# Optimization experiments

Hardware: AMD Instinct MI355X
Metric: run time of the kernel (lower is better)

## Reference

```python
import jax, jax.numpy as jnp
import numpy as np

B, NQ, T, D, H, L = 2, 4, 1024, 1024, 16, 8
CARD, N_COND, COND_D, WIN = 1024, 64, 768, 5
DFF = 4 * D


def _ln(x, g, b):
    m = jnp.mean(x, axis=-1, keepdims=True)
    v = jnp.var(x, axis=-1, keepdims=True)
    return (x - m) * jax.lax.rsqrt(v + 1e-5) * g + b


def _mha(qx, kx, vx, Wq, bq, Wk, bk, Wv, bv, Wo, bo, mask):
    # qx:(B,Tq,D) kx/vx:(B,Tk,*)
    Bq, Tq = qx.shape[0], qx.shape[1]
    Tk = kx.shape[1]
    hd = D // H
    q = (qx @ Wq + bq).reshape(Bq, Tq, H, hd)
    k = (kx @ Wk + bk).reshape(Bq, Tk, H, hd)
    v = (vx @ Wv + bv).reshape(Bq, Tk, H, hd)
    s = jnp.einsum('bthd,bshd->bhts', q, k) / jnp.sqrt(jnp.float32(hd))
    if mask is not None:
        s = s + mask  # additive banded mask (0 in-band, -inf outside)
    p = jax.nn.softmax(s, axis=-1)
    o = jnp.einsum('bhts,bshd->bthd', p, v).reshape(Bq, Tq, D)
    return o @ Wo + bo


def _pos_emb(t, d):
    # matches get_sinusoidal_positional_embeddings: interleaved sin/cos
    i = jnp.arange(d // 2, dtype=jnp.float32) * 2.0
    p = jnp.arange(t, dtype=jnp.float32)[:, None]
    theta = p / (10000.0 ** (i / d))[None, :]  # (t, d/2)
    return jnp.stack([jnp.sin(theta), jnp.cos(theta)], axis=-1).reshape(t, d)[None]


def _band_mask(t, w):
    # magnet_restricted_att_mask with shift=0: log(tril(triu(1, -w), w))
    idx = jnp.arange(t)
    dlt = idx[None, :] - idx[:, None]
    return jnp.where((dlt >= -w) & (dlt <= w), 0.0, -jnp.inf).astype(jnp.float32)


def _forward(x, cond, emb,
             ln1_g, ln1_b, sWq, sbq, sWk, sbk, sWv, sbv, sWo, sbo,
             ln2_g, ln2_b, cWq, cbq, cWk, cbk, cWv, cbv, cWo, cbo,
             ln3_g, ln3_b, W1, b1, W2, b2, out_g, out_b, headW, headb):
    # multi-codebook embedding sum: (B,NQ,T) -> (B,T,D)
    h = emb[0][x[:, 0]]
    for q in range(1, NQ):
        h = h + emb[q][x[:, q]]
    h = h + _pos_emb(T, D).astype(h.dtype)
    mask = _band_mask(T, WIN)
    for l in range(L):
        sin = _ln(h, ln1_g[l], ln1_b[l])
        h = h + _mha(sin, sin, sin, sWq[l], sbq[l], sWk[l], sbk[l],
                     sWv[l], sbv[l], sWo[l], sbo[l], mask)
        cin = _ln(h, ln2_g[l], ln2_b[l])
        h = h + _mha(cin, cond, cond, cWq[l], cbq[l], cWk[l], cbk[l],
                     cWv[l], cbv[l], cWo[l], cbo[l], None)
        fin = _ln(h, ln3_g[l], ln3_b[l])
        h = h + (jax.nn.gelu(fin @ W1[l] + b1[l], approximate=True) @ W2[l] + b2[l])
    h = _ln(h, out_g, out_b)
    # per-codebook heads -> (B, NQ, T, CARD)
    return jnp.einsum('btd,qdk->bqtk', h, headW) + headb[None, :, None, :]


def setup_inputs() -> dict:
    key = jax.random.key(0)
    ks = iter(jax.random.split(key, 40))
    s = 0.02
    nrm = lambda shape: jax.random.normal(next(ks), shape, dtype=jnp.float32) * s
    inp = {}
    inp['x'] = jax.random.randint(next(ks), (B, NQ, T), 0, CARD + 1)
    inp['cond'] = jax.random.normal(next(ks), (B, N_COND, COND_D), dtype=jnp.float32)
    inp['emb'] = nrm((NQ, CARD + 1, D))
    for nm in ('ln1', 'ln2', 'ln3'):
        inp[nm + '_g'] = jnp.ones((L, D), jnp.float32)
        inp[nm + '_b'] = jnp.zeros((L, D), jnp.float32)
    # self-attn projections
    inp['sWq'], inp['sWk'], inp['sWv'], inp['sWo'] = (nrm((L, D, D)) for _ in range(4))
    inp['sbq'] = jnp.zeros((L, D), jnp.float32); inp['sbk'] = jnp.zeros((L, D), jnp.float32)
    inp['sbv'] = jnp.zeros((L, D), jnp.float32); inp['sbo'] = jnp.zeros((L, D), jnp.float32)
    # cross-attn projections (k/v act on cond_dim)
    inp['cWq'] = nrm((L, D, D)); inp['cWk'] = nrm((L, COND_D, D))
    inp['cWv'] = nrm((L, COND_D, D)); inp['cWo'] = nrm((L, D, D))
    inp['cbq'] = jnp.zeros((L, D), jnp.float32); inp['cbk'] = jnp.zeros((L, D), jnp.float32)
    inp['cbv'] = jnp.zeros((L, D), jnp.float32); inp['cbo'] = jnp.zeros((L, D), jnp.float32)
    inp['W1'] = nrm((L, D, DFF)); inp['b1'] = jnp.zeros((L, DFF), jnp.float32)
    inp['W2'] = nrm((L, DFF, D)); inp['b2'] = jnp.zeros((L, D), jnp.float32)
    inp['out_g'] = jnp.ones((D,), jnp.float32); inp['out_b'] = jnp.zeros((D,), jnp.float32)
    inp['headW'] = nrm((NQ, D, CARD)); inp['headb'] = jnp.zeros((NQ, CARD), jnp.float32)
    return inp


def reference(x, cond, emb,
              ln1_g, ln1_b, sWq, sbq, sWk, sbk, sWv, sbv, sWo, sbo,
              ln2_g, ln2_b, cWq, cbq, cWk, cbk, cWv, cbv, cWo, cbo,
              ln3_g, ln3_b, W1, b1, W2, b2, out_g, out_b, headW, headb):
    return _forward(x, cond, emb,
                    ln1_g, ln1_b, sWq, sbq, sWk, sbk, sWv, sbv, sWo, sbo,
                    ln2_g, ln2_b, cWq, cbq, cWk, cbk, cWv, cbv, cWo, cbo,
                    ln3_g, ln3_b, W1, b1, W2, b2, out_g, out_b, headW, headb)
```

## Files before the change

kernel.cpp:

```cpp
#include <hip/hip_runtime.h>
#include <math.h>

#define BATCH   2
#define NQ_CB   4
#define T_SEQ   1024
#define DMODEL  1024
#define NHEAD   16
#define HDIM    64
#define NLAYER  8
#define CARD_SZ 1024
#define NCOND   64
#define CONDD   768
#define DFF_SZ  4096
#define WIN     5

typedef __attribute__((ext_vector_type(8))) short bf16x8;
typedef __attribute__((ext_vector_type(4))) float f32x4;
typedef unsigned short ushortx;

__device__ inline short f2bf(float f) {
  union { float f; unsigned u; } c;
  c.f = f;
  unsigned r = (c.u + 0x7FFFu + ((c.u >> 16) & 1u)) >> 16;
  return (short)r;
}
__device__ inline float bf2f(unsigned short u) {
  union { unsigned u; float f; } c;
  c.u = ((unsigned)u) << 16;
  return c.f;
}

__device__ inline void gld_lds16(const void* g, void* s) {
  __builtin_amdgcn_global_load_lds(
      (const __attribute__((address_space(1))) void*)g,
      (__attribute__((address_space(3))) void*)s, 16, 0, 0);
}

__global__ __launch_bounds__(256) void pack_kernel(
    const float* __restrict__ src, short* __restrict__ dst, int K, int N)
{
  size_t matoff = (size_t)blockIdx.z * K * N;
  src += matoff; dst += matoff;
  int gid = blockIdx.x * 256 + threadIdx.x;
  int slab = gid >> 6, cell = gid & 63;
  int KT = K >> 5;
  int ng = slab / KT, kt = slab - ng * KT;
  int n = ng * 16 + (cell & 15);
  int k = kt * 32 + (cell >> 4) * 8;
  bf16x8 pk;
#pragma unroll
  for (int j = 0; j < 8; ++j) pk[j] = f2bf(src[(size_t)(k + j) * N + n]);
  *(bf16x8*)&dst[(size_t)gid * 8] = pk;
}

__global__ __launch_bounds__(256) void embed_kernel(
    const int* __restrict__ x, const float* __restrict__ emb,
    float* __restrict__ h)
{
  int bt = blockIdx.x;
  int b = bt >> 10, t = bt & (T_SEQ - 1);
  int tid = threadIdx.x;
  float4 acc = make_float4(0.f, 0.f, 0.f, 0.f);
#pragma unroll
  for (int q = 0; q < NQ_CB; ++q) {
    int idx = x[(b * NQ_CB + q) * T_SEQ + t];
    const float4* er =
        (const float4*)(emb + ((size_t)q * (CARD_SZ + 1) + idx) * DMODEL);
    float4 e = er[tid];
    acc.x += e.x; acc.y += e.y; acc.z += e.z; acc.w += e.w;
  }
  int d0 = tid * 4;
  float c = -logf(10000.f) * (2.f / (float)DMODEL);
  float th0 = (float)t * expf(c * (float)(d0 >> 1));
  float th1 = (float)t * expf(c * (float)((d0 + 2) >> 1));
  acc.x += sinf(th0); acc.y += cosf(th0);
  acc.z += sinf(th1); acc.w += cosf(th1);
  ((float4*)(h + (size_t)bt * DMODEL))[tid] = acc;
}

__global__ __launch_bounds__(256) void ln_kernel(
    const float* __restrict__ x, const float* __restrict__ g,
    const float* __restrict__ b, ushortx* __restrict__ y)
{
  int row = blockIdx.x;
  int tid = threadIdx.x;
  const float4* xr = (const float4*)(x + (size_t)row * DMODEL);
  float4 v = xr[tid];
  float s  = v.x + v.y + v.z + v.w;
  float ss = v.x * v.x + v.y * v.y + v.z * v.z + v.w * v.w;
#pragma unroll
  for (int off = 32; off; off >>= 1) {
    s  += __shfl_xor(s, off, 64);
    ss += __shfl_xor(ss, off, 64);
  }
  __shared__ float sh_s[4], sh_ss[4];
  int w = tid >> 6;
  if ((tid & 63) == 0) { sh_s[w] = s; sh_ss[w] = ss; }
  __syncthreads();
  s  = sh_s[0] + sh_s[1] + sh_s[2] + sh_s[3];
  ss = sh_ss[0] + sh_ss[1] + sh_ss[2] + sh_ss[3];
  float mean = s * (1.f / DMODEL);
  float var  = ss * (1.f / DMODEL) - mean * mean;
  float rstd = rsqrtf(var + 1e-5f);
  float4 gv = ((const float4*)g)[tid];
  float4 bv = ((const float4*)b)[tid];
  ushort4 o;
  o.x = (ushortx)f2bf((v.x - mean) * rstd * gv.x + bv.x);
  o.y = (ushortx)f2bf((v.y - mean) * rstd * gv.y + bv.y);
  o.z = (ushortx)f2bf((v.z - mean) * rstd * gv.z + bv.z);
  o.w = (ushortx)f2bf((v.w - mean) * rstd * gv.w + bv.w);
  *(ushort4*)(y + (size_t)row * DMODEL + tid * 4) = o;
}

#define FL_GELU  1
#define FL_REMAP 2
#define FL_OBF16 4

template <int MW, int ABF16>
__global__ __launch_bounds__(256, 2) void gemm_pk(
    const void* __restrict__ Ain,
    const short* __restrict__ Wp0, const short* __restrict__ Wp1,
    const short* __restrict__ Wp2, long wstride, int nw,
    const float* __restrict__ b0, const float* __restrict__ b1,
    const float* __restrict__ b2, long bstride,
    const float* __restrict__ resid,
    void* __restrict__ C0v, void* __restrict__ C1v, void* __restrict__ C2v,
    long cstride,
    int M, int N, int K, int flags)
{
  const int BM = MW * 32;
  __shared__ __align__(16) short Als[BM * 32];
  __shared__ __align__(16) short Bls[128 * 32];

  int tid = threadIdx.x;
  int z = blockIdx.z;
  int w = z % nw, li = z / nw;
  const short* Wp = (w == 0 ? Wp0 : (w == 1 ? Wp1 : Wp2)) + (size_t)li * wstride;
  const float* bias = (w == 0 ? b0 : (w == 1 ? b1 : b2)) + (size_t)li * bstride;
  char* Cb = (char*)(w == 0 ? C0v : (w == 1 ? C1v : C2v)) + (size_t)li * cstride;

  int bm = blockIdx.y * BM;
  int bn = blockIdx.x * 128;
  int wave = tid >> 6, lane = tid & 63;
  int wm = (wave >> 1) * (MW * 16);
  int wn = (wave & 1) * 64;
  int KT = K >> 5;

  f32x4 acc[MW][4];
#pragma unroll
  for (int i = 0; i < MW; ++i)
#pragma unroll
    for (int j = 0; j < 4; ++j) {
      acc[i][j][0] = 0.f; acc[i][j][1] = 0.f;
      acc[i][j][2] = 0.f; acc[i][j][3] = 0.f;
    }

  for (int kt = 0; kt < KT; ++kt) {
    int k0 = kt * 32;
#pragma unroll
    for (int i = 0; i < 2; ++i) {
      int g = wave * 2 + i;
      const short* src = Wp + ((size_t)((bn >> 4) + g) * KT + kt) * 512 + lane * 8;
      gld_lds16(src, &Bls[g * 512]);
    }
    if (ABF16) {
      const ushortx* A16 = (const ushortx*)Ain;
#pragma unroll
      for (int i = 0; i < (MW * 2 + 3) / 4; ++i) {
        int g = wave + i * 4;
        if (g < MW * 2) {
          const ushortx* src =
              A16 + (size_t)(bm + g * 16 + (lane & 15)) * K + k0 + (lane >> 4) * 8;
          gld_lds16(src, &Als[g * 512]);
        }
      }
    } else {
      const float* Af = (const float*)Ain;
      int m = tid >> 2, k8 = tid & 3;
      const float* src = Af + (size_t)(bm + m) * K + k0 + k8 * 8;
      float4 f0 = *(const float4*)src;
      float4 f1 = *(const float4*)(src + 4);
      bf16x8 pk;
      pk[0] = f2bf(f0.x); pk[1] = f2bf(f0.y); pk[2] = f2bf(f0.z); pk[3] = f2bf(f0.w);
      pk[4] = f2bf(f1.x); pk[5] = f2bf(f1.y); pk[6] = f2bf(f1.z); pk[7] = f2bf(f1.w);
      *(bf16x8*)&Als[(m >> 4) * 512 + (((m & 15) | (k8 << 4)) * 8)] = pk;
    }
    __syncthreads();

    bf16x8 af[MW], bfr[4];
#pragma unroll
    for (int i = 0; i < MW; ++i)
      af[i] = *(bf16x8*)&Als[((wm >> 4) + i) * 512 + lane * 8];
#pragma unroll
    for (int j = 0; j < 4; ++j)
      bfr[j] = *(bf16x8*)&Bls[((wn >> 4) + j) * 512 + lane * 8];
#pragma unroll
    for (int i = 0; i < MW; ++i)
#pragma unroll
      for (int j = 0; j < 4; ++j)
        acc[i][j] = __builtin_amdgcn_mfma_f32_16x16x32_bf16(
            af[i], bfr[j], acc[i][j], 0, 0, 0);
    __syncthreads();
  }

  int quad = lane >> 4, col = lane & 15;
#pragma unroll
  for (int i = 0; i < MW; ++i) {
    int m0 = bm + wm + i * 16 + quad * 4;
#pragma unroll
    for (int j = 0; j < 4; ++j) {
      int n0 = bn + wn + j * 16 + col;
      float bval = bias[n0];
#pragma unroll
      for (int r = 0; r < 4; ++r) {
        int m = m0 + r;
        float v = acc[i][j][r] + bval;
        if (flags & FL_GELU) {
          v = 0.5f * v *
              (1.f + tanhf(0.7978845608028654f * (v + 0.044715f * v * v * v)));
        }
        if (resid) v += resid[(size_t)m * N + n0];
        size_t row;
        if (flags & FL_REMAP)
          row = ((size_t)(m >> 10) * NQ_CB + li) * T_SEQ + (m & (T_SEQ - 1));
        else
          row = m;
        if (flags & FL_OBF16)
          ((ushortx*)Cb)[row * N + n0] = (ushortx)f2bf(v);
        else
          ((float*)Cb)[row * N + n0] = v;
      }
    }
  }
}

__global__ __launch_bounds__(256) void self_attn_kernel(
    const ushortx* __restrict__ q, const ushortx* __restrict__ k,
    const ushortx* __restrict__ v, ushortx* __restrict__ o)
{
  int w = blockIdx.x * 4 + (threadIdx.x >> 6);
  int lane = threadIdx.x & 63;
  int t = w & (T_SEQ - 1);
  int bh = w >> 10;
  int h = bh & (NHEAD - 1);
  int b = bh >> 4;
  size_t base = ((size_t)(b * T_SEQ) * DMODEL) + h * HDIM + lane;
  float qv = bf2f(q[base + (size_t)t * DMODEL]);

  float sc[2 * WIN + 1];
  float mx = -1e30f;
#pragma unroll
  for (int j = 0; j < 2 * WIN + 1; ++j) {
    int s = t - WIN + j;
    float d;
    if (s >= 0 && s < T_SEQ) {
      float kv = bf2f(k[base + (size_t)s * DMODEL]);
      d = qv * kv;
#pragma unroll
      for (int off = 32; off; off >>= 1) d += __shfl_xor(d, off, 64);
      d *= 0.125f;
    } else {
      d = -1e30f;
    }
    sc[j] = d;
    mx = fmaxf(mx, d);
  }
  float sum = 0.f;
#pragma unroll
  for (int j = 0; j < 2 * WIN + 1; ++j) {
    sc[j] = expf(sc[j] - mx);
    sum += sc[j];
  }
  float inv = 1.f / sum;
  float ov = 0.f;
#pragma unroll
  for (int j = 0; j < 2 * WIN + 1; ++j) {
    int s = t - WIN + j;
    if (s >= 0 && s < T_SEQ) ov += sc[j] * bf2f(v[base + (size_t)s * DMODEL]);
  }
  o[base + (size_t)t * DMODEL] = (ushortx)f2bf(ov * inv);
}

__global__ __launch_bounds__(256) void cross_attn_kernel(
    const ushortx* __restrict__ q, const ushortx* __restrict__ k,
    const ushortx* __restrict__ v, ushortx* __restrict__ o)
{
  int w = blockIdx.x * 4 + (threadIdx.x >> 6);
  int lane = threadIdx.x & 63;
  int t = w & (T_SEQ - 1);
  int h = (w >> 10) & (NHEAD - 1);
  int b = w >> 14;
  size_t qoff = ((size_t)(b * T_SEQ + t) * DMODEL) + h * HDIM;
  float qv = bf2f(q[qoff + lane]);

  const ushortx* krow = k + ((size_t)(b * NCOND + lane) * DMODEL) + h * HDIM;
  float s_l = 0.f;
#pragma unroll
  for (int d = 0; d < HDIM; ++d) {
    float qd = __shfl(qv, d, 64);
    s_l += qd * bf2f(krow[d]);
  }
  s_l *= 0.125f;
  float m = s_l;
#pragma unroll
  for (int off = 32; off; off >>= 1) m = fmaxf(m, __shfl_xor(m, off, 64));
  float p = expf(s_l - m);
  float sum = p;
#pragma unroll
  for (int off = 32; off; off >>= 1) sum += __shfl_xor(sum, off, 64);
  p /= sum;

  float ov = 0.f;
  const ushortx* vb = v + ((size_t)(b * NCOND) * DMODEL) + h * HDIM + lane;
#pragma unroll
  for (int s = 0; s < NCOND; ++s) {
    float ps = __shfl(p, s, 64);
    ov += ps * bf2f(vb[(size_t)s * DMODEL]);
  }
  o[qoff + lane] = (ushortx)f2bf(ov);
}

static void gemm_launch(hipStream_t st, int MW, int abf16,
    const void* A, const short* W0, const short* W1, const short* W2,
    long wstride, int nw,
    const float* b0, const float* b1, const float* b2, long bstride,
    const float* resid, void* C0, void* C1, void* C2, long cstride,
    int M, int N, int K, int z, int flags)
{
  dim3 grid(N / 128, M / (MW * 32), z);
  if (MW == 4)
    hipLaunchKernelGGL((gemm_pk<4, 1>), grid, dim3(256), 0, st, A, W0, W1, W2,
                       wstride, nw, b0, b1, b2, bstride, resid, C0, C1, C2,
                       cstride, M, N, K, flags);
  else if (abf16)
    hipLaunchKernelGGL((gemm_pk<2, 1>), grid, dim3(256), 0, st, A, W0, W1, W2,
                       wstride, nw, b0, b1, b2, bstride, resid, C0, C1, C2,
                       cstride, M, N, K, flags);
  else
    hipLaunchKernelGGL((gemm_pk<2, 0>), grid, dim3(256), 0, st, A, W0, W1, W2,
                       wstride, nw, b0, b1, b2, bstride, resid, C0, C1, C2,
                       cstride, M, N, K, flags);
}

extern "C" void kernel_launch(void* const* d_in, const int* in_sizes, int n_in,
                              void* d_out, int out_size, void* d_ws, size_t ws_size,
                              hipStream_t stream)
{
  const int*   x     = (const int*)  d_in[0];
  const float* cond  = (const float*)d_in[1];
  const float* emb   = (const float*)d_in[2];
  const float* ln1_g = (const float*)d_in[3];
  const float* ln1_b = (const float*)d_in[4];
  const float* ln2_g = (const float*)d_in[5];
  const float* ln2_b = (const float*)d_in[6];
  const float* ln3_g = (const float*)d_in[7];
  const float* ln3_b = (const float*)d_in[8];
  const float* sWq   = (const float*)d_in[9];
  const float* sWk   = (const float*)d_in[10];
  const float* sWv   = (const float*)d_in[11];
  const float* sWo   = (const float*)d_in[12];
  const float* sbq   = (const float*)d_in[13];
  const float* sbk   = (const float*)d_in[14];
  const float* sbv   = (const float*)d_in[15];
  const float* sbo   = (const float*)d_in[16];
  const float* cWq   = (const float*)d_in[17];
  const float* cWk   = (const float*)d_in[18];
  const float* cWv   = (const float*)d_in[19];
  const float* cWo   = (const float*)d_in[20];
  const float* cbq   = (const float*)d_in[21];
  const float* cbk   = (const float*)d_in[22];
  const float* cbv   = (const float*)d_in[23];
  const float* cbo   = (const float*)d_in[24];
  const float* W1    = (const float*)d_in[25];
  const float* b1    = (const float*)d_in[26];
  const float* W2    = (const float*)d_in[27];
  const float* b2    = (const float*)d_in[28];
  const float* out_g = (const float*)d_in[29];
  const float* out_b = (const float*)d_in[30];
  const float* headW = (const float*)d_in[31];
  const float* headb = (const float*)d_in[32];

  float* out = (float*)d_out;
  const size_t MB = 1u << 20;
  const long MAT = 1048576L;
  const long CMAT = 768L * 1024;
  const long FMAT = 4L * 1048576;
  const int M = BATCH * T_SEQ;

  char* wsb = (char*)d_ws;
  float*   h   = (float*)(wsb);
  ushortx* tmp = (ushortx*)(wsb + 8 * MB);
  ushortx* qb  = (ushortx*)(wsb + 12 * MB);
  ushortx* kb  = (ushortx*)(wsb + 16 * MB);
  ushortx* vb  = (ushortx*)(wsb + 20 * MB);
  ushortx* ao  = (ushortx*)(wsb + 24 * MB);
  ushortx* ffn = qb;
  ushortx* ckv = (ushortx*)(wsb + 28 * MB);
  short*   PB  = (short*)(wsb + 32 * MB);

  bool big = ws_size >= (size_t)32 * MB + (size_t)268435456;

  auto pack = [&](const float* src, short* dst, int K, int N, int z) {
    hipLaunchKernelGGL(pack_kernel, dim3((unsigned)((size_t)K * N / 2048), 1, z),
                       dim3(256), 0, stream, src, dst, K, N);
  };

  short *Pq = PB, *Pk = PB + 8 * MAT, *Pv = PB + 16 * MAT, *Po = PB + 24 * MAT;
  short *Pcq = PB + 32 * MAT, *Pco = PB + 40 * MAT;
  short *Pck = PB + 48 * MAT, *Pcv = PB + 54 * MAT;
  short *Pw1 = PB + 60 * MAT, *Pw2 = PB + 92 * MAT, *Phd = PB + 124 * MAT;
  if (big) {
    pack(sWq, Pq, 1024, 1024, 8);  pack(sWk, Pk, 1024, 1024, 8);
    pack(sWv, Pv, 1024, 1024, 8);  pack(sWo, Po, 1024, 1024, 8);
    pack(cWq, Pcq, 1024, 1024, 8); pack(cWo, Pco, 1024, 1024, 8);
    pack(cWk, Pck, 768, 1024, 8);  pack(cWv, Pcv, 768, 1024, 8);
    pack(W1, Pw1, 1024, 4096, 8);  pack(W2, Pw2, 4096, 1024, 8);
    pack(headW, Phd, 1024, 1024, 4);
  }

  hipLaunchKernelGGL(embed_kernel, dim3(M), dim3(256), 0, stream, x, emb, h);

  if (big) {
    gemm_launch(stream, 2, 0, cond, Pck, Pcv, nullptr, CMAT, 2,
                cbk, cbv, nullptr, 1024, nullptr,
                ckv, (char*)ckv + 262144, nullptr, 524288,
                BATCH * NCOND, DMODEL, CONDD, 16, FL_OBF16);
  } else {
    pack(cWk, PB, 768, 1024, 8);
    gemm_launch(stream, 2, 0, cond, PB, nullptr, nullptr, CMAT, 1,
                cbk, nullptr, nullptr, 1024, nullptr,
                ckv, nullptr, nullptr, 524288,
                BATCH * NCOND, DMODEL, CONDD, 8, FL_OBF16);
    pack(cWv, PB, 768, 1024, 8);
    gemm_launch(stream, 2, 0, cond, PB, nullptr, nullptr, CMAT, 1,
                cbv, nullptr, nullptr, 1024, nullptr,
                (char*)ckv + 262144, nullptr, nullptr, 524288,
                BATCH * NCOND, DMODEL, CONDD, 8, FL_OBF16);
  }

  const int attn_blocks = BATCH * NHEAD * T_SEQ / 4;

  for (int l = 0; l < NLAYER; ++l) {
    const float* L1g = ln1_g + l * DMODEL, *L1b = ln1_b + l * DMODEL;
    const float* L2g = ln2_g + l * DMODEL, *L2b = ln2_b + l * DMODEL;
    const float* L3g = ln3_g + l * DMODEL, *L3b = ln3_b + l * DMODEL;

    hipLaunchKernelGGL(ln_kernel, dim3(M), dim3(256), 0, stream, h, L1g, L1b, tmp);
    {
      const short *wq, *wk, *wv;
      if (big) { wq = Pq + l * MAT; wk = Pk + l * MAT; wv = Pv + l * MAT; }
      else {
        pack(sWq + (size_t)l * MAT, PB, 1024, 1024, 1);
        pack(sWk + (size_t)l * MAT, PB + MAT, 1024, 1024, 1);
        pack(sWv + (size_t)l * MAT, PB + 2 * MAT, 1024, 1024, 1);
        wq = PB; wk = PB + MAT; wv = PB + 2 * MAT;
      }
      gemm_launch(stream, 4, 1, tmp, wq, wk, wv, 0, 3,
                  sbq + l * DMODEL, sbk + l * DMODEL, sbv + l * DMODEL, 0,
                  nullptr, qb, kb, vb, 0, M, DMODEL, DMODEL, 3, FL_OBF16);
    }
    hipLaunchKernelGGL(self_attn_kernel, dim3(attn_blocks), dim3(256), 0, stream,
                       qb, kb, vb, ao);
    {
      const short* wo = big ? Po + l * MAT : PB;
      if (!big) pack(sWo + (size_t)l * MAT, PB, 1024, 1024, 1);
      gemm_launch(stream, 2, 1, ao, wo, nullptr, nullptr, 0, 1,
                  sbo + l * DMODEL, nullptr, nullptr, 0,
                  h, h, nullptr, nullptr, 0, M, DMODEL, DMODEL, 1, 0);
    }

    hipLaunchKernelGGL(ln_kernel, dim3(M), dim3(256), 0, stream, h, L2g, L2b, tmp);
    {
      const short* wcq = big ? Pcq + l * MAT : PB;
      if (!big) pack(cWq + (size_t)l * MAT, PB, 1024, 1024, 1);
      gemm_launch(stream, 2, 1, tmp, wcq, nullptr, nullptr, 0, 1,
                  cbq + l * DMODEL, nullptr, nullptr, 0,
                  nullptr, qb, nullptr, nullptr, 0, M, DMODEL, DMODEL, 1, FL_OBF16);
    }
    hipLaunchKernelGGL(cross_attn_kernel, dim3(attn_blocks), dim3(256), 0, stream,
                       qb, ckv + (size_t)(2 * l) * 131072,
                       ckv + (size_t)(2 * l + 1) * 131072, ao);
    {
      const short* wco = big ? Pco + l * MAT : PB;
      if (!big) pack(cWo + (size_t)l * MAT, PB, 1024, 1024, 1);
      gemm_launch(stream, 2, 1, ao, wco, nullptr, nullptr, 0, 1,
                  cbo + l * DMODEL, nullptr, nullptr, 0,
                  h, h, nullptr, nullptr, 0, M, DMODEL, DMODEL, 1, 0);
    }

    hipLaunchKernelGGL(ln_kernel, dim3(M), dim3(256), 0, stream, h, L3g, L3b, tmp);
    {
      const short* w1p = big ? Pw1 + l * FMAT : PB;
      if (!big) pack(W1 + (size_t)l * FMAT, PB, 1024, 4096, 1);
      gemm_launch(stream, 4, 1, tmp, w1p, nullptr, nullptr, 0, 1,
                  b1 + l * DFF_SZ, nullptr, nullptr, 0,
                  nullptr, ffn, nullptr, nullptr, 0,
                  M, DFF_SZ, DMODEL, 1, FL_GELU | FL_OBF16);
      const short* w2p = big ? Pw2 + l * FMAT : PB;
      if (!big) pack(W2 + (size_t)l * FMAT, PB, 4096, 1024, 1);
      gemm_launch(stream, 2, 1, ffn, w2p, nullptr, nullptr, 0, 1,
                  b2 + l * DMODEL, nullptr, nullptr, 0,
                  h, h, nullptr, nullptr, 0, M, DMODEL, DFF_SZ, 1, 0);
    }
  }

  hipLaunchKernelGGL(ln_kernel, dim3(M), dim3(256), 0, stream, h, out_g, out_b, tmp);
  {
    const short* whd = big ? Phd : PB;
    if (!big) pack(headW, PB, 1024, 1024, 4);
    gemm_launch(stream, 4, 1, tmp, whd, nullptr, nullptr, MAT, 1,
                headb, nullptr, nullptr, CARD_SZ, nullptr,
                out, nullptr, nullptr, 0, M, CARD_SZ, DMODEL, 4, FL_REMAP);
  }
}
```

Before: 3.896 ms.

## Double-buffer GEMM LDS tiles with async prefetch and 64-wide K steps

Restructures the packed-weight GEMM main loop into a two-stage pipeline. The next K tile is issued with global_load_lds into a second LDS buffer, and only the older stage is waited on through an explicit vmcnt count. The K step per iteration doubles to 64, which halves the number of barriers. The aim is to hide global-load latency behind MFMA work. The cost is twice the LDS footprint, and the fp32-A path still waits for all loads, so it overlaps little.

```diff
diff --git a/kernel.cpp b/kernel.cpp
--- a/kernel.cpp
+++ b/kernel.cpp
@@ -34,6 +34,16 @@
   __builtin_amdgcn_global_load_lds(
       (const __attribute__((address_space(1))) void*)g,
       (__attribute__((address_space(3))) void*)s, 16, 0, 0);
+}
+
+template <int N> __device__ inline void s_wait_vmcnt() {
+  asm volatile("s_waitcnt vmcnt(%0)" :: "n"(N) : "memory");
+}
+
+__device__ inline void blk_bar() {
+  asm volatile("" ::: "memory");
+  __builtin_amdgcn_s_barrier();
+  asm volatile("" ::: "memory");
 }
 
 __global__ __launch_bounds__(256) void pack_kernel(
@@ -128,9 +138,8 @@
     long cstride,
     int M, int N, int K, int flags)
 {
-  const int BM = MW * 32;
-  __shared__ __align__(16) short Als[BM * 32];
-  __shared__ __align__(16) short Bls[128 * 32];
+  __shared__ __align__(16) short Als[2][MW * 2048];
+  __shared__ __align__(16) short Bls[2][8192];
 
   int tid = threadIdx.x;
   int z = blockIdx.z;
@@ -139,12 +148,14 @@
   const float* bias = (w == 0 ? b0 : (w == 1 ? b1 : b2)) + (size_t)li * bstride;
   char* Cb = (char*)(w == 0 ? C0v : (w == 1 ? C1v : C2v)) + (size_t)li * cstride;
 
-  int bm = blockIdx.y * BM;
+  int bm = blockIdx.y * (MW * 32);
   int bn = blockIdx.x * 128;
   int wave = tid >> 6, lane = tid & 63;
   int wm = (wave >> 1) * (MW * 16);
   int wn = (wave & 1) * 64;
   int KT = K >> 5;
+  const int NT = K >> 6;
+  constexpr int NSTG = 4 + (ABF16 ? MW : 0);
 
   f32x4 acc[MW][4];
 #pragma unroll
@@ -155,52 +166,73 @@
       acc[i][j][2] = 0.f; acc[i][j][3] = 0.f;
     }
 
-  for (int kt = 0; kt < KT; ++kt) {
-    int k0 = kt * 32;
-#pragma unroll
-    for (int i = 0; i < 2; ++i) {
-      int g = wave * 2 + i;
-      const short* src = Wp + ((size_t)((bn >> 4) + g) * KT + kt) * 512 + lane * 8;
-      gld_lds16(src, &Bls[g * 512]);
+  auto stage = [&](int kt, int buf) {
+#pragma unroll
+    for (int i = 0; i < 4; ++i) {
+      int s = wave * 4 + i;
+      const short* src =
+          Wp + ((size_t)((bn >> 4) + (s >> 1)) * KT + 2 * kt + (s & 1)) * 512 +
+          lane * 8;
+      gld_lds16(src, &Bls[buf][s * 512]);
     }
     if (ABF16) {
       const ushortx* A16 = (const ushortx*)Ain;
 #pragma unroll
-      for (int i = 0; i < (MW * 2 + 3) / 4; ++i) {
-        int g = wave + i * 4;
-        if (g < MW * 2) {
-          const ushortx* src =
-              A16 + (size_t)(bm + g * 16 + (lane & 15)) * K + k0 + (lane >> 4) * 8;
-          gld_lds16(src, &Als[g * 512]);
-        }
+      for (int i = 0; i < MW; ++i) {
+        int s = wave * MW + i;
+        const ushortx* src = A16 +
+            (size_t)(bm + (s >> 1) * 16 + (lane & 15)) * K +
+            kt * 64 + (s & 1) * 32 + (lane >> 4) * 8;
+        gld_lds16(src, &Als[buf][s * 512]);
       }
     } else {
       const float* Af = (const float*)Ain;
-      int m = tid >> 2, k8 = tid & 3;
-      const float* src = Af + (size_t)(bm + m) * K + k0 + k8 * 8;
-      float4 f0 = *(const float4*)src;
-      float4 f1 = *(const float4*)(src + 4);
-      bf16x8 pk;
-      pk[0] = f2bf(f0.x); pk[1] = f2bf(f0.y); pk[2] = f2bf(f0.z); pk[3] = f2bf(f0.w);
-      pk[4] = f2bf(f1.x); pk[5] = f2bf(f1.y); pk[6] = f2bf(f1.z); pk[7] = f2bf(f1.w);
-      *(bf16x8*)&Als[(m >> 4) * 512 + (((m & 15) | (k8 << 4)) * 8)] = pk;
-    }
-    __syncthreads();
-
-    bf16x8 af[MW], bfr[4];
-#pragma unroll
-    for (int i = 0; i < MW; ++i)
-      af[i] = *(bf16x8*)&Als[((wm >> 4) + i) * 512 + lane * 8];
-#pragma unroll
-    for (int j = 0; j < 4; ++j)
-      bfr[j] = *(bf16x8*)&Bls[((wn >> 4) + j) * 512 + lane * 8];
-#pragma unroll
-    for (int i = 0; i < MW; ++i)
+      int m = tid >> 2, kq = tid & 3;
+#pragma unroll
+      for (int ks = 0; ks < 2; ++ks) {
+        const float* src = Af + (size_t)(bm + m) * K + kt * 64 + ks * 32 + kq * 8;
+        float4 f0 = *(const float4*)src;
+        float4 f1 = *(const float4*)(src + 4);
+        bf16x8 pk;
+        pk[0] = f2bf(f0.x); pk[1] = f2bf(f0.y); pk[2] = f2bf(f0.z); pk[3] = f2bf(f0.w);
+        pk[4] = f2bf(f1.x); pk[5] = f2bf(f1.y); pk[6] = f2bf(f1.z); pk[7] = f2bf(f1.w);
+        *(bf16x8*)&Als[buf][((m >> 4) * 2 + ks) * 512 + ((m & 15) | (kq << 4)) * 8] = pk;
+      }
+    }
+  };
+
+  stage(0, 0);
+  int cur = 0;
+
+  for (int kt = 0; kt < NT; ++kt) {
+    if (kt + 1 < NT) {
+      stage(kt + 1, cur ^ 1);
+      if (ABF16) s_wait_vmcnt<NSTG>();
+      else       s_wait_vmcnt<0>();
+    } else {
+      s_wait_vmcnt<0>();
+    }
+    if (!ABF16) asm volatile("s_waitcnt lgkmcnt(0)" ::: "memory");
+    blk_bar();
+
+#pragma unroll
+    for (int ks = 0; ks < 2; ++ks) {
+      bf16x8 af[MW], bfr[4];
+#pragma unroll
+      for (int i = 0; i < MW; ++i)
+        af[i] = *(bf16x8*)&Als[cur][(((wm >> 4) + i) * 2 + ks) * 512 + lane * 8];
 #pragma unroll
       for (int j = 0; j < 4; ++j)
-        acc[i][j] = __builtin_amdgcn_mfma_f32_16x16x32_bf16(
-            af[i], bfr[j], acc[i][j], 0, 0, 0);
-    __syncthreads();
+        bfr[j] = *(bf16x8*)&Bls[cur][(((wn >> 4) + j) * 2 + ks) * 512 + lane * 8];
+#pragma unroll
+      for (int i = 0; i < MW; ++i)
+#pragma unroll
+        for (int j = 0; j < 4; ++j)
+          acc[i][j] = __builtin_amdgcn_mfma_f32_16x16x32_bf16(
+              af[i], bfr[j], acc[i][j], 0, 0, 0);
+    }
+    blk_bar();
+    cur ^= 1;
   }
 
   int quad = lane >> 4, col = lane & 15;
```

Measured after the change: 3.373 ms. 1.16x faster.
